# Kernel optimization log

Hardware: AMD Instinct MI355X
Metric: run time of the kernel (lower is better)

## Reference

```python
import jax, jax.numpy as jnp
import numpy as np

N_HEADS = 16


def setup_inputs() -> dict:
    key = jax.random.key(0)
    k_x, k_len, k_pos, k_attn, k_proj = jax.random.split(key, 5)
    B, W, c, C = 4, 256, 32, 1024
    x = jax.random.normal(k_x, (B, W, c, C), dtype=jnp.float32)
    # ragged word lengths in [1, c]; left-aligned padding mask as in pad()
    lengths = jax.random.randint(k_len, (B, W), 1, c + 1)
    attention_mask = (jnp.arange(c)[None, None, :] < lengths[:, :, None]).astype(jnp.int32)
    pos_emb = jax.random.normal(k_pos, (W, C), dtype=jnp.float32) * 0.02
    attn_w = jax.random.normal(k_attn, (C, 3 * C), dtype=jnp.float32) * (C ** -0.5)
    proj_w = jax.random.normal(k_proj, (C, C), dtype=jnp.float32) * (C ** -0.5)
    return {"x": x, "attention_mask": attention_mask, "pos_emb": pos_emb,
            "attn_w": attn_w, "proj_w": proj_w}


def reference(x, attention_mask, pos_emb, attn_w, proj_w):
    # first_time=True path of CharAttention.forward (eval mode: dropout = identity)
    B, W, c, C = x.shape
    H = N_HEADS
    hd = C // H
    last_ix = jnp.sum(attention_mask, axis=2) - 1          # [B, W]

    qkv = jnp.einsum('bwce,ef->bwcf', x, attn_w)            # [B, W, c, 3C]
    q, k, v = jnp.split(qkv, 3, axis=-1)
    # [B, W, c, C] -> [B, W, H, c, hd]
    def to_heads(t):
        return t.reshape(B, W, c, H, hd).transpose(0, 1, 3, 2, 4)
    q, k, v = to_heads(q), to_heads(k), to_heads(v)

    scale = 1.0 / jnp.sqrt(jnp.asarray(hd, dtype=x.dtype))
    scores = jnp.einsum('bwhqd,bwhkd->bwhqk', q, k) * scale  # [B, W, H, c, c]
    causal = jnp.tril(jnp.ones((c, c), dtype=bool))
    scores = jnp.where(causal[None, None, None], scores, jnp.finfo(x.dtype).min)
    attn = jax.nn.softmax(scores, axis=-1)
    o = jnp.einsum('bwhqk,bwhkd->bwhqd', attn, v)            # [B, W, H, c, hd]
    o = o.transpose(0, 1, 3, 2, 4).reshape(B, W, c, C)       # [B, W, c, C]

    # gather the last real-character position of each word
    idx = last_ix[:, :, None, None]                          # [B, W, 1, 1]
    gathered = jnp.take_along_axis(o, idx, axis=2)[:, :, 0, :]  # [B, W, C]

    out = gathered + pos_emb[None, :, :]
    out = jnp.einsum('bwe,ef->bwf', out, proj_w)
    return out
```

## Files before the change

kernel.cpp:

```cpp
#include <hip/hip_runtime.h>
#include <hip/hip_bf16.h>
#include <stdint.h>

typedef __attribute__((ext_vector_type(8))) short short8;
typedef __attribute__((ext_vector_type(4))) float floatx4;

#define GPTR(p) (const __attribute__((address_space(1))) void*)(p)
#define LPTR(p) (__attribute__((address_space(3))) void*)(p)

__device__ __forceinline__ ushort f2bf(float f) {
    union { float f; uint32_t u; } v; v.f = f;
    uint32_t u = v.u;
    uint32_t r = (u + 0x7FFFu + ((u >> 16) & 1u)) >> 16;
    return (ushort)r;
}
__device__ __forceinline__ float bf2f(ushort b) {
    union { uint32_t u; float f; } v; v.u = ((uint32_t)b) << 16;
    return v.f;
}

__global__ void prep_kernel(const int* __restrict__ mask, int* __restrict__ lastix,
                            int* __restrict__ row_start, int* __restrict__ mc) {
    __shared__ int wsum[16];
    int tid = threadIdx.x;
    int wave = tid >> 6, lane = tid & 63;
    const int4* m4 = (const int4*)(mask + (size_t)tid * 32);
    int s = 0;
    #pragma unroll
    for (int i = 0; i < 8; ++i) { int4 v = m4[i]; s += v.x + v.y + v.z + v.w; }
    lastix[tid] = s - 1;
    int scan = s;
    #pragma unroll
    for (int off = 1; off < 64; off <<= 1) {
        int v = __shfl_up(scan, off);
        if (lane >= off) scan += v;
    }
    if (lane == 63) wsum[wave] = scan;
    __syncthreads();
    int base = 0;
    for (int w = 0; w < wave; ++w) base += wsum[w];
    int incl = base + scan;
    row_start[tid] = incl - s;
    if (tid == 1023) mc[0] = incl;
}

__global__ void gather_kernel(const float* __restrict__ x, const int* __restrict__ lastix,
                              const int* __restrict__ row_start,
                              ushort* __restrict__ xc, ushort* __restrict__ xq) {
    int bw = blockIdx.x;
    int t  = lastix[bw];
    int rs = row_start[bw];
    const float4* src = (const float4*)(x + (size_t)bw * 32 * 1024);
    int n4 = (t + 1) * 256;
    for (int i = threadIdx.x; i < n4; i += 256) {
        float4 v = src[i];
        ushort4 o; o.x = f2bf(v.x); o.y = f2bf(v.y); o.z = f2bf(v.z); o.w = f2bf(v.w);
        int j = i >> 8, c4 = i & 255;
        ((ushort4*)(xc + (size_t)(rs + j) * 1024))[c4] = o;
        if (j == t) ((ushort4*)(xq + (size_t)bw * 1024))[c4] = o;
    }
}

__global__ void wcvt_kernel(const float* __restrict__ attn_w, const float* __restrict__ proj_w,
                            ushort* __restrict__ wqT, ushort* __restrict__ wk,
                            ushort* __restrict__ wvT, ushort* __restrict__ wpT) {
    __shared__ float tile[32][33];
    int bx = blockIdx.x;
    int r0 = blockIdx.y * 32;
    int tx = threadIdx.x, ty = threadIdx.y;
    if (bx >= 96) {
        int c0 = (bx - 96) * 32;
        for (int i = ty; i < 32; i += 8)
            wk[(size_t)(r0 + i) * 1024 + c0 + tx] =
                f2bf(attn_w[(size_t)(r0 + i) * 3072 + 1024 + c0 + tx]);
        return;
    }
    const float* src; ushort* dst; int N, csrc0, c0;
    if (bx < 32)      { src = attn_w; dst = wqT; N = 3072; c0 = bx * 32;        csrc0 = c0; }
    else if (bx < 64) { src = attn_w; dst = wvT; N = 3072; c0 = (bx - 32) * 32; csrc0 = 2048 + c0; }
    else              { src = proj_w; dst = wpT; N = 1024; c0 = (bx - 64) * 32; csrc0 = c0; }
    for (int i = ty; i < 32; i += 8)
        tile[i][tx] = src[(size_t)(r0 + i) * N + csrc0 + tx];
    __syncthreads();
    for (int i = ty; i < 32; i += 8)
        dst[(size_t)(c0 + i) * 1024 + r0 + tx] = f2bf(tile[tx][i]);
}

template <bool OUT_BF16>
__global__ __launch_bounds__(256)
void gemm128_kernel(const ushort* __restrict__ A, int lda, long sA,
                    const ushort* __restrict__ Bt, int ldb, long sB,
                    void* __restrict__ C, int ldc, long sC, int K) {
    __shared__ ushort As[128 * 32];
    __shared__ ushort Bs[128 * 32];

    const int bm = blockIdx.x, bn = blockIdx.y, z = blockIdx.z;
    A  += (size_t)z * sA;
    Bt += (size_t)z * sB;

    const int tid  = threadIdx.x;
    const int wave = tid >> 6;
    const int lane = tid & 63;
    const int wm = wave & 1, wn = wave >> 1;
    const int quad = lane >> 4, l15 = lane & 15;

    floatx4 acc[4][4] = {};

    const int arow = bm * 128 + wave * 16 + (lane >> 2);
    const int brow = bn * 128 + wave * 16 + (lane >> 2);
    const int kcol = (lane & 3) * 8;

    for (int kt = 0; kt < K; kt += 32) {
        #pragma unroll
        for (int iss = 0; iss < 2; ++iss) {
            const ushort* gA = A  + (size_t)(arow + iss * 64) * lda + kt + kcol;
            const ushort* gB = Bt + (size_t)(brow + iss * 64) * ldb + kt + kcol;
            ushort* lA = As + (iss * 64 + wave * 16) * 32;
            ushort* lB = Bs + (iss * 64 + wave * 16) * 32;
            __builtin_amdgcn_global_load_lds(GPTR(gA), LPTR(lA), 16, 0, 0);
            __builtin_amdgcn_global_load_lds(GPTR(gB), LPTR(lB), 16, 0, 0);
        }
        __syncthreads();

        short8 af[4], bf[4];
        #pragma unroll
        for (int i = 0; i < 4; ++i)
            af[i] = *(const short8*)&As[(wm * 64 + i * 16 + l15) * 32 + quad * 8];
        #pragma unroll
        for (int j = 0; j < 4; ++j)
            bf[j] = *(const short8*)&Bs[(wn * 64 + j * 16 + l15) * 32 + quad * 8];
        #pragma unroll
        for (int i = 0; i < 4; ++i)
            #pragma unroll
            for (int j = 0; j < 4; ++j)
                acc[i][j] = __builtin_amdgcn_mfma_f32_16x16x32_bf16(af[i], bf[j], acc[i][j], 0, 0, 0);
        __syncthreads();
    }

    #pragma unroll
    for (int i = 0; i < 4; ++i) {
        #pragma unroll
        for (int j = 0; j < 4; ++j) {
            int r0 = bm * 128 + wm * 64 + i * 16 + quad * 4;
            int c  = bn * 128 + wn * 64 + j * 16 + l15;
            #pragma unroll
            for (int r = 0; r < 4; ++r) {
                float v = acc[i][j][r];
                size_t idx = (size_t)z * sC + (size_t)(r0 + r) * ldc + c;
                if (OUT_BF16) ((ushort*)C)[idx] = f2bf(v);
                else          ((float*) C)[idx] = v;
            }
        }
    }
}

template <bool OUT_BF16, bool ADD_POS>
__global__ __launch_bounds__(256)
void gemm64_kernel(const ushort* __restrict__ A, int lda, long sA,
                   const ushort* __restrict__ Bt, int ldb, long sB,
                   void* __restrict__ C, int ldc, int cColPerZ, int K,
                   const float* __restrict__ pos) {
    __shared__ ushort As[64 * 32];
    __shared__ ushort Bs[64 * 32];

    const int bm = blockIdx.x, bn = blockIdx.y, z = blockIdx.z;
    A  += (size_t)z * sA;
    Bt += (size_t)z * sB;

    const int tid  = threadIdx.x;
    const int wave = tid >> 6;
    const int lane = tid & 63;
    const int wm = wave & 1, wn = wave >> 1;
    const int quad = lane >> 4, l15 = lane & 15;

    floatx4 acc[2][2] = {};

    const int srow = wave * 16 + (lane >> 2);
    const int kcol = (lane & 3) * 8;

    for (int kt = 0; kt < K; kt += 32) {
        const ushort* gA = A  + (size_t)(bm * 64 + srow) * lda + kt + kcol;
        const ushort* gB = Bt + (size_t)(bn * 64 + srow) * ldb + kt + kcol;
        ushort* lA = As + (wave * 16) * 32;
        ushort* lB = Bs + (wave * 16) * 32;
        __builtin_amdgcn_global_load_lds(GPTR(gA), LPTR(lA), 16, 0, 0);
        __builtin_amdgcn_global_load_lds(GPTR(gB), LPTR(lB), 16, 0, 0);
        __syncthreads();

        short8 af[2], bf[2];
        #pragma unroll
        for (int i = 0; i < 2; ++i)
            af[i] = *(const short8*)&As[(wm * 32 + i * 16 + l15) * 32 + quad * 8];
        #pragma unroll
        for (int j = 0; j < 2; ++j)
            bf[j] = *(const short8*)&Bs[(wn * 32 + j * 16 + l15) * 32 + quad * 8];
        #pragma unroll
        for (int i = 0; i < 2; ++i)
            #pragma unroll
            for (int j = 0; j < 2; ++j)
                acc[i][j] = __builtin_amdgcn_mfma_f32_16x16x32_bf16(af[i], bf[j], acc[i][j], 0, 0, 0);
        __syncthreads();
    }

    #pragma unroll
    for (int i = 0; i < 2; ++i) {
        #pragma unroll
        for (int j = 0; j < 2; ++j) {
            int r0 = bm * 64 + wm * 32 + i * 16 + quad * 4;
            int cc = z * cColPerZ + bn * 64 + wn * 32 + j * 16 + l15;
            #pragma unroll
            for (int r = 0; r < 4; ++r) {
                float v = acc[i][j][r];
                if (ADD_POS) v += pos[(size_t)((r0 + r) & 255) * 1024 + cc];
                size_t idx = (size_t)(r0 + r) * ldc + cc;
                if (OUT_BF16) ((ushort*)C)[idx] = f2bf(v);
                else          ((float*) C)[idx] = v;
            }
        }
    }
}

__global__ __launch_bounds__(256)
void attn2_kernel(const ushort* __restrict__ xc, const ushort* __restrict__ U,
                  const int* __restrict__ lastix, const int* __restrict__ row_start,
                  ushort* __restrict__ Z) {
    __shared__ ushort Xs[32 * 1032];
    __shared__ ushort Us[16 * 1032];
    __shared__ float  Ss[16 * 33];
    __shared__ float  Ps[32 * 16];

    const int bw = blockIdx.x;
    const int tid = threadIdx.x;
    const int t  = lastix[bw];
    const int rs = row_start[bw];
    const int wave = tid >> 6, lane = tid & 63;
    const int quad = lane >> 4, l15 = lane & 15;

    const ushort* xsrc = xc + (size_t)rs * 1024;
    int nv = (t + 1) * 128;
    for (int i = tid; i < nv; i += 256) {
        int j = i >> 7, c = i & 127;
        *(short8*)&Xs[j * 1032 + c * 8] = *(const short8*)&xsrc[i * 8];
    }
    for (int i = tid; i < 16 * 128; i += 256) {
        int h = i >> 7, c = i & 127;
        *(short8*)&Us[h * 1032 + c * 8] =
            *(const short8*)&U[(size_t)h * 1048576 + (size_t)bw * 1024 + c * 8];
    }
    __syncthreads();

    if (wave < 2) {
        floatx4 acc = {0.f, 0.f, 0.f, 0.f};
        int arow = wave * 16 + l15;
        for (int kt = 0; kt < 1024; kt += 32) {
            short8 a = *(const short8*)&Xs[arow * 1032 + kt + quad * 8];
            short8 b = *(const short8*)&Us[l15  * 1032 + kt + quad * 8];
            acc = __builtin_amdgcn_mfma_f32_16x16x32_bf16(a, b, acc, 0, 0, 0);
        }
        #pragma unroll
        for (int r = 0; r < 4; ++r)
            Ss[l15 * 33 + wave * 16 + quad * 4 + r] = acc[r] * 0.125f;
    }
    __syncthreads();

    if (wave == 0) {
        float s[8]; float mx = -1e30f;
        #pragma unroll
        for (int r = 0; r < 8; ++r) {
            int j = quad * 8 + r;
            float v = Ss[l15 * 33 + j];
            v = (j <= t) ? v : -1e30f;
            s[r] = v; mx = fmaxf(mx, v);
        }
        mx = fmaxf(mx, __shfl_xor(mx, 16));
        mx = fmaxf(mx, __shfl_xor(mx, 32));
        float l = 0.f;
        #pragma unroll
        for (int r = 0; r < 8; ++r) { s[r] = __expf(s[r] - mx); l += s[r]; }
        l += __shfl_xor(l, 16);
        l += __shfl_xor(l, 32);
        float inv = 1.f / l;
        #pragma unroll
        for (int r = 0; r < 8; ++r)
            Ps[(quad * 8 + r) * 16 + l15] = s[r] * inv;
    }
    __syncthreads();

    float z[16][4];
    #pragma unroll
    for (int h = 0; h < 16; ++h)
        #pragma unroll
        for (int c = 0; c < 4; ++c) z[h][c] = 0.f;
    const int e0 = tid * 4;
    for (int j = 0; j <= t; ++j) {
        float4 p0 = *(const float4*)&Ps[j * 16 + 0];
        float4 p1 = *(const float4*)&Ps[j * 16 + 4];
        float4 p2 = *(const float4*)&Ps[j * 16 + 8];
        float4 p3 = *(const float4*)&Ps[j * 16 + 12];
        float pr[16] = {p0.x, p0.y, p0.z, p0.w, p1.x, p1.y, p1.z, p1.w,
                        p2.x, p2.y, p2.z, p2.w, p3.x, p3.y, p3.z, p3.w};
        ushort4 xv = *(const ushort4*)&Xs[j * 1032 + e0];
        float xf[4] = {bf2f(xv.x), bf2f(xv.y), bf2f(xv.z), bf2f(xv.w)};
        #pragma unroll
        for (int h = 0; h < 16; ++h)
            #pragma unroll
            for (int c = 0; c < 4; ++c)
                z[h][c] += pr[h] * xf[c];
    }
    #pragma unroll
    for (int h = 0; h < 16; ++h) {
        ushort4 o;
        o.x = f2bf(z[h][0]); o.y = f2bf(z[h][1]);
        o.z = f2bf(z[h][2]); o.w = f2bf(z[h][3]);
        *(ushort4*)&Z[(size_t)h * 1048576 + (size_t)bw * 1024 + e0] = o;
    }
}

extern "C" void kernel_launch(void* const* d_in, const int* in_sizes, int n_in,
                              void* d_out, int out_size, void* d_ws, size_t ws_size,
                              hipStream_t stream) {
    const float* x        = (const float*)d_in[0];
    const int*   mask     = (const int*)  d_in[1];
    const float* pos_emb  = (const float*)d_in[2];
    const float* attn_w   = (const float*)d_in[3];
    const float* proj_w   = (const float*)d_in[4];
    float*       out      = (float*)d_out;

    const long MB2 = 1048576;

    char* ws = (char*)d_ws;
    size_t off = 0;
    ushort* xc_bf = (ushort*)(ws + off); off += (size_t)32768 * 1024 * 2;
    ushort* U_bf  = (ushort*)(ws + off); off += (size_t)16 * MB2 * 2;
    ushort* Z_bf  = (ushort*)(ws + off); off += (size_t)16 * MB2 * 2;
    ushort* wqT   = (ushort*)(ws + off); off += MB2 * 2;
    ushort* wk    = (ushort*)(ws + off); off += MB2 * 2;
    ushort* wvT   = (ushort*)(ws + off); off += MB2 * 2;
    ushort* wpT   = (ushort*)(ws + off); off += MB2 * 2;
    ushort* xq_bf = (ushort*)(ws + off); off += MB2 * 2;
    ushort* q_bf  = (ushort*)(ws + off); off += MB2 * 2;
    ushort* y_bf  = (ushort*)(ws + off); off += MB2 * 2;
    int*    lastix= (int*)   (ws + off); off += 4096;
    int*    rowst = (int*)   (ws + off); off += 4096;
    int*    mc    = (int*)   (ws + off); off += 256;

    prep_kernel<<<1, 1024, 0, stream>>>(mask, lastix, rowst, mc);

    wcvt_kernel<<<dim3(128, 32), dim3(32, 8), 0, stream>>>(attn_w, proj_w, wqT, wk, wvT, wpT);

    gather_kernel<<<1024, 256, 0, stream>>>(x, lastix, rowst, xc_bf, xq_bf);

    gemm64_kernel<true, false><<<dim3(16, 16, 1), 256, 0, stream>>>(
        xq_bf, 1024, 0, wqT, 1024, 0, (void*)q_bf, 1024, 0, 1024, nullptr);

    gemm128_kernel<true><<<dim3(8, 8, 16), 256, 0, stream>>>(
        q_bf, 1024, 64, wk, 1024, 64, (void*)U_bf, 1024, MB2, 64);

    attn2_kernel<<<1024, 256, 0, stream>>>(xc_bf, U_bf, lastix, rowst, Z_bf);

    gemm64_kernel<true, true><<<dim3(16, 1, 16), 256, 0, stream>>>(
        Z_bf, 1024, MB2, wvT, 1024, 65536, (void*)y_bf, 1024, 64, 1024, pos_emb);

    gemm64_kernel<false, false><<<dim3(16, 16, 1), 256, 0, stream>>>(
        y_bf, 1024, 0, wpT, 1024, 0, (void*)out, 1024, 0, 1024, nullptr);
}
```

Measured before the change: 315.1 us.

## Fuse char gather into attention kernel and split-K the square GEMMs

Removes the prep and gather kernels and the compacted bf16 copy of x. The attention kernel now computes each word's length from the mask and reads and converts fp32 x rows directly into LDS. A small qrow kernel extracts only the query rows. The U and Z buffers are re-laid out word-major so per-word reads are contiguous. The two 1024x1024x1024 GEMMs become 4-way split-K with an fp32 partial buffer plus a combine kernel, raising block count from 256 to 1024. This trades an extra combine launch and partial-sum traffic for better occupancy, and drops a full write and re-read of the compacted activations.

```diff
diff --git a/kernel.cpp b/kernel.cpp
--- a/kernel.cpp
+++ b/kernel.cpp
@@ -19,46 +19,23 @@
     return v.f;
 }
 
-__global__ void prep_kernel(const int* __restrict__ mask, int* __restrict__ lastix,
-                            int* __restrict__ row_start, int* __restrict__ mc) {
-    __shared__ int wsum[16];
-    int tid = threadIdx.x;
-    int wave = tid >> 6, lane = tid & 63;
-    const int4* m4 = (const int4*)(mask + (size_t)tid * 32);
-    int s = 0;
-    #pragma unroll
-    for (int i = 0; i < 8; ++i) { int4 v = m4[i]; s += v.x + v.y + v.z + v.w; }
-    lastix[tid] = s - 1;
-    int scan = s;
-    #pragma unroll
-    for (int off = 1; off < 64; off <<= 1) {
-        int v = __shfl_up(scan, off);
-        if (lane >= off) scan += v;
-    }
-    if (lane == 63) wsum[wave] = scan;
-    __syncthreads();
-    int base = 0;
-    for (int w = 0; w < wave; ++w) base += wsum[w];
-    int incl = base + scan;
-    row_start[tid] = incl - s;
-    if (tid == 1023) mc[0] = incl;
-}
-
-__global__ void gather_kernel(const float* __restrict__ x, const int* __restrict__ lastix,
-                              const int* __restrict__ row_start,
-                              ushort* __restrict__ xc, ushort* __restrict__ xq) {
-    int bw = blockIdx.x;
-    int t  = lastix[bw];
-    int rs = row_start[bw];
-    const float4* src = (const float4*)(x + (size_t)bw * 32 * 1024);
-    int n4 = (t + 1) * 256;
-    for (int i = threadIdx.x; i < n4; i += 256) {
-        float4 v = src[i];
-        ushort4 o; o.x = f2bf(v.x); o.y = f2bf(v.y); o.z = f2bf(v.z); o.w = f2bf(v.w);
-        int j = i >> 8, c4 = i & 255;
-        ((ushort4*)(xc + (size_t)(rs + j) * 1024))[c4] = o;
-        if (j == t) ((ushort4*)(xq + (size_t)bw * 1024))[c4] = o;
-    }
+__global__ void qrow_kernel(const float* __restrict__ x, const int* __restrict__ mask,
+                            ushort* __restrict__ xq) {
+    __shared__ int t_sh;
+    int bw = blockIdx.x, tid = threadIdx.x;
+    if (tid < 32) {
+        int s = mask[bw * 32 + tid];
+        #pragma unroll
+        for (int off = 16; off; off >>= 1) s += __shfl_xor(s, off);
+        if (tid == 0) t_sh = s - 1;
+    }
+    __syncthreads();
+    int t = t_sh;
+    const float4* src = (const float4*)(x + ((size_t)bw * 32 + t) * 1024);
+    float4 v = src[tid];
+    ushort4 o;
+    o.x = f2bf(v.x); o.y = f2bf(v.y); o.z = f2bf(v.z); o.w = f2bf(v.w);
+    ((ushort4*)(xq + (size_t)bw * 1024))[tid] = o;
 }
 
 __global__ void wcvt_kernel(const float* __restrict__ attn_w, const float* __restrict__ proj_w,
@@ -86,6 +63,82 @@
         dst[(size_t)(c0 + i) * 1024 + r0 + tx] = f2bf(tile[tx][i]);
 }
 
+__global__ __launch_bounds__(256)
+void gemm64sk_kernel(const ushort* __restrict__ A, const ushort* __restrict__ Bt,
+                     float* __restrict__ Cpart) {
+    __shared__ ushort As[64 * 32];
+    __shared__ ushort Bs[64 * 32];
+
+    const int bm = blockIdx.x, bn = blockIdx.y, z = blockIdx.z;
+    const int kofs = z * 256;
+
+    const int tid  = threadIdx.x;
+    const int wave = tid >> 6;
+    const int lane = tid & 63;
+    const int wm = wave & 1, wn = wave >> 1;
+    const int quad = lane >> 4, l15 = lane & 15;
+
+    floatx4 acc[2][2] = {};
+
+    const int srow = wave * 16 + (lane >> 2);
+    const int kcol = (lane & 3) * 8;
+
+    for (int kt = 0; kt < 256; kt += 32) {
+        const ushort* gA = A  + (size_t)(bm * 64 + srow) * 1024 + kofs + kt + kcol;
+        const ushort* gB = Bt + (size_t)(bn * 64 + srow) * 1024 + kofs + kt + kcol;
+        ushort* lA = As + (wave * 16) * 32;
+        ushort* lB = Bs + (wave * 16) * 32;
+        __builtin_amdgcn_global_load_lds(GPTR(gA), LPTR(lA), 16, 0, 0);
+        __builtin_amdgcn_global_load_lds(GPTR(gB), LPTR(lB), 16, 0, 0);
+        __syncthreads();
+
+        short8 af[2], bf[2];
+        #pragma unroll
+        for (int i = 0; i < 2; ++i)
+            af[i] = *(const short8*)&As[(wm * 32 + i * 16 + l15) * 32 + quad * 8];
+        #pragma unroll
+        for (int j = 0; j < 2; ++j)
+            bf[j] = *(const short8*)&Bs[(wn * 32 + j * 16 + l15) * 32 + quad * 8];
+        #pragma unroll
+        for (int i = 0; i < 2; ++i)
+            #pragma unroll
+            for (int j = 0; j < 2; ++j)
+                acc[i][j] = __builtin_amdgcn_mfma_f32_16x16x32_bf16(af[i], bf[j], acc[i][j], 0, 0, 0);
+        __syncthreads();
+    }
+
+    #pragma unroll
+    for (int i = 0; i < 2; ++i) {
+        #pragma unroll
+        for (int j = 0; j < 2; ++j) {
+            int r0 = bm * 64 + wm * 32 + i * 16 + quad * 4;
+            int c  = bn * 64 + wn * 32 + j * 16 + l15;
+            #pragma unroll
+            for (int r = 0; r < 4; ++r)
+                Cpart[(size_t)z * 1048576 + (size_t)(r0 + r) * 1024 + c] = acc[i][j][r];
+        }
+    }
+}
+
+template <bool OUT_BF16>
+__global__ void combine4_kernel(const float* __restrict__ P, void* __restrict__ C) {
+    int i = blockIdx.x * 256 + threadIdx.x;
+    const float4* p = (const float4*)P;
+    float4 a = p[i], b = p[i + 262144], c = p[i + 524288], d = p[i + 786432];
+    float4 s;
+    s.x = a.x + b.x + c.x + d.x;
+    s.y = a.y + b.y + c.y + d.y;
+    s.z = a.z + b.z + c.z + d.z;
+    s.w = a.w + b.w + c.w + d.w;
+    if (OUT_BF16) {
+        ushort4 o;
+        o.x = f2bf(s.x); o.y = f2bf(s.y); o.z = f2bf(s.z); o.w = f2bf(s.w);
+        ((ushort4*)C)[i] = o;
+    } else {
+        ((float4*)C)[i] = s;
+    }
+}
+
 template <bool OUT_BF16>
 __global__ __launch_bounds__(256)
 void gemm128_kernel(const ushort* __restrict__ A, int lda, long sA,
@@ -221,31 +274,40 @@
 }
 
 __global__ __launch_bounds__(256)
-void attn2_kernel(const ushort* __restrict__ xc, const ushort* __restrict__ U,
-                  const int* __restrict__ lastix, const int* __restrict__ row_start,
-                  ushort* __restrict__ Z) {
+void attn2_kernel(const float* __restrict__ x, const int* __restrict__ mask,
+                  const ushort* __restrict__ U, ushort* __restrict__ Z) {
     __shared__ ushort Xs[32 * 1032];
     __shared__ ushort Us[16 * 1032];
     __shared__ float  Ss[16 * 33];
     __shared__ float  Ps[32 * 16];
+    __shared__ int    t_sh;
 
     const int bw = blockIdx.x;
     const int tid = threadIdx.x;
-    const int t  = lastix[bw];
-    const int rs = row_start[bw];
     const int wave = tid >> 6, lane = tid & 63;
     const int quad = lane >> 4, l15 = lane & 15;
 
-    const ushort* xsrc = xc + (size_t)rs * 1024;
-    int nv = (t + 1) * 128;
-    for (int i = tid; i < nv; i += 256) {
-        int j = i >> 7, c = i & 127;
-        *(short8*)&Xs[j * 1032 + c * 8] = *(const short8*)&xsrc[i * 8];
-    }
+    if (tid < 32) {
+        int s = mask[bw * 32 + tid];
+        #pragma unroll
+        for (int off = 16; off; off >>= 1) s += __shfl_xor(s, off);
+        if (tid == 0) t_sh = s - 1;
+    }
+    __syncthreads();
+    const int t = t_sh;
+
+    const float4* xsrc = (const float4*)(x + (size_t)bw * 32 * 1024);
+    int n4 = (t + 1) * 256;
+    for (int i = tid; i < n4; i += 256) {
+        float4 v = xsrc[i];
+        int j = i >> 8, c4 = i & 255;
+        ushort4 o; o.x = f2bf(v.x); o.y = f2bf(v.y); o.z = f2bf(v.z); o.w = f2bf(v.w);
+        *(ushort4*)&Xs[j * 1032 + c4 * 4] = o;
+    }
+    const ushort* ubase = U + (size_t)bw * 16384;
     for (int i = tid; i < 16 * 128; i += 256) {
         int h = i >> 7, c = i & 127;
-        *(short8*)&Us[h * 1032 + c * 8] =
-            *(const short8*)&U[(size_t)h * 1048576 + (size_t)bw * 1024 + c * 8];
+        *(short8*)&Us[h * 1032 + c * 8] = *(const short8*)&ubase[i * 8];
     }
     __syncthreads();
 
@@ -312,7 +374,7 @@
         ushort4 o;
         o.x = f2bf(z[h][0]); o.y = f2bf(z[h][1]);
         o.z = f2bf(z[h][2]); o.w = f2bf(z[h][3]);
-        *(ushort4*)&Z[(size_t)h * 1048576 + (size_t)bw * 1024 + e0] = o;
+        *(ushort4*)&Z[(size_t)bw * 16384 + h * 1024 + e0] = o;
     }
 }
 
@@ -330,9 +392,10 @@
 
     char* ws = (char*)d_ws;
     size_t off = 0;
-    ushort* xc_bf = (ushort*)(ws + off); off += (size_t)32768 * 1024 * 2;
     ushort* U_bf  = (ushort*)(ws + off); off += (size_t)16 * MB2 * 2;
     ushort* Z_bf  = (ushort*)(ws + off); off += (size_t)16 * MB2 * 2;
+    float*  qpart = (float*) (ws + off); off += (size_t)4 * MB2 * 4;
+    float*  opart = (float*) (ws + off); off += (size_t)4 * MB2 * 4;
     ushort* wqT   = (ushort*)(ws + off); off += MB2 * 2;
     ushort* wk    = (ushort*)(ws + off); off += MB2 * 2;
     ushort* wvT   = (ushort*)(ws + off); off += MB2 * 2;
@@ -340,27 +403,22 @@
     ushort* xq_bf = (ushort*)(ws + off); off += MB2 * 2;
     ushort* q_bf  = (ushort*)(ws + off); off += MB2 * 2;
     ushort* y_bf  = (ushort*)(ws + off); off += MB2 * 2;
-    int*    lastix= (int*)   (ws + off); off += 4096;
-    int*    rowst = (int*)   (ws + off); off += 4096;
-    int*    mc    = (int*)   (ws + off); off += 256;
-
-    prep_kernel<<<1, 1024, 0, stream>>>(mask, lastix, rowst, mc);
+
+    qrow_kernel<<<1024, 256, 0, stream>>>(x, mask, xq_bf);
 
     wcvt_kernel<<<dim3(128, 32), dim3(32, 8), 0, stream>>>(attn_w, proj_w, wqT, wk, wvT, wpT);
 
-    gather_kernel<<<1024, 256, 0, stream>>>(x, lastix, rowst, xc_bf, xq_bf);
-
-    gemm64_kernel<true, false><<<dim3(16, 16, 1), 256, 0, stream>>>(
-        xq_bf, 1024, 0, wqT, 1024, 0, (void*)q_bf, 1024, 0, 1024, nullptr);
+    gemm64sk_kernel<<<dim3(16, 16, 4), 256, 0, stream>>>(xq_bf, wqT, qpart);
+    combine4_kernel<true><<<1024, 256, 0, stream>>>(qpart, (void*)q_bf);
 
     gemm128_kernel<true><<<dim3(8, 8, 16), 256, 0, stream>>>(
-        q_bf, 1024, 64, wk, 1024, 64, (void*)U_bf, 1024, MB2, 64);
-
-    attn2_kernel<<<1024, 256, 0, stream>>>(xc_bf, U_bf, lastix, rowst, Z_bf);
+        q_bf, 1024, 64, wk, 1024, 64, (void*)U_bf, 16384, 1024, 64);
+
+    attn2_kernel<<<1024, 256, 0, stream>>>(x, mask, U_bf, Z_bf);
 
     gemm64_kernel<true, true><<<dim3(16, 1, 16), 256, 0, stream>>>(
-        Z_bf, 1024, MB2, wvT, 1024, 65536, (void*)y_bf, 1024, 64, 1024, pos_emb);
-
-    gemm64_kernel<false, false><<<dim3(16, 16, 1), 256, 0, stream>>>(
-        y_bf, 1024, 0, wpT, 1024, 0, (void*)out, 1024, 0, 1024, nullptr);
-}
+        Z_bf, 16384, 1024, wvT, 1024, 65536, (void*)y_bf, 1024, 64, 1024, pos_emb);
+
+    gemm64sk_kernel<<<dim3(16, 16, 4), 256, 0, stream>>>(y_bf, wpT, opart);
+    combine4_kernel<false><<<1024, 256, 0, stream>>>(opart, (void*)out);
+}
```

Measured after the change: 321.0 us. Within noise of the previous version (+1.9%).
